# Optimization experiments

Measured on AMD Instinct MI355X. Metric: run time of the kernel, lower is better.

Reference implementation:

```python
import jax, jax.numpy as jnp
import numpy as np

N_NODES = 50000
N_EDGES = 800000
IN_CH = 128
HID = 16
HEADS = 8
OUT_CH = 40
NEG_SLOPE = 0.2  # PyG GATConv default leaky_relu slope


def segment_softmax(logits, seg, num_segments):
    # logits: [E, H], softmax over edges sharing the same destination node
    m = jax.ops.segment_max(logits, seg, num_segments=num_segments)  # [N, H]
    e = jnp.exp(logits - m[seg])
    s = jax.ops.segment_sum(e, seg, num_segments=num_segments)  # [N, H]
    return e / s[seg]


def gat_conv(x, edge_index, W, att_src, att_dst, bias, heads, ch, concat):
    N = x.shape[0]
    h = (x @ W).reshape(N, heads, ch)                     # [N, H, C]
    a_src = jnp.sum(h * att_src, axis=-1)                 # [N, H]
    a_dst = jnp.sum(h * att_dst, axis=-1)                 # [N, H]
    src, dst = edge_index[0], edge_index[1]
    alpha = jax.nn.leaky_relu(a_src[src] + a_dst[dst], NEG_SLOPE)  # [E, H]
    alpha = segment_softmax(alpha, dst, N)                # [E, H]
    msg = h[src] * alpha[:, :, None]                      # [E, H, C]
    out = jax.ops.segment_sum(msg, dst, num_segments=N)   # [N, H, C]
    out = out.reshape(N, heads * ch) if concat else out.mean(axis=1)
    return out + bias


def setup_inputs() -> dict:
    key = jax.random.key(0)
    ks = jax.random.split(key, 10)
    g = 0.1
    return {
        "x": jax.random.normal(ks[0], (N_NODES, IN_CH), jnp.float32),
        "edge_index": jax.random.randint(ks[1], (2, N_EDGES), 0, N_NODES, jnp.int32),
        "W1": jax.random.normal(ks[2], (IN_CH, HEADS * HID), jnp.float32) * g,
        "att_src1": jax.random.normal(ks[3], (HEADS, HID), jnp.float32) * g,
        "att_dst1": jax.random.normal(ks[4], (HEADS, HID), jnp.float32) * g,
        "b1": jnp.zeros((HEADS * HID,), jnp.float32),
        "W2": jax.random.normal(ks[5], (HEADS * HID, OUT_CH), jnp.float32) * g,
        "att_src2": jax.random.normal(ks[6], (1, OUT_CH), jnp.float32) * g,
        "att_dst2": jax.random.normal(ks[7], (1, OUT_CH), jnp.float32) * g,
        "b2": jnp.zeros((OUT_CH,), jnp.float32),
    }


def reference(x, edge_index, W1, att_src1, att_dst1, b1, W2, att_src2, att_dst2, b2):
    # layer 1: GATConv(in->hid, heads=8, concat) + ELU (dropout is identity in eval)
    h = gat_conv(x, edge_index, W1, att_src1, att_dst1, b1, HEADS, HID, concat=True)
    h = jax.nn.elu(h)
    # layer 2: GATConv(hid*heads->out, heads=1, concat=False)
    out = gat_conv(h, edge_index, W2, att_src2, att_dst2, b2, 1, OUT_CH, concat=False)
    return out
```

## Files before the change

kernel.cpp:

```cpp
#include <hip/hip_runtime.h>
#include <hip/hip_bf16.h>
#include <math.h>

#define N_NODES 50000
#define E_EDGES 800000
#define IN_CH 128
#define HIDX 128
#define OUT_CH 40
#define NEG_SLOPE 0.2f
#define RANK_BLKS 160
#define EDGES_PER_RANK_BLK 5000
#define GEMM_BLKS_X 782
#define PAD_SHIFT 6

static __device__ __forceinline__ unsigned int f2bf_pk(float lo, float hi) {
    unsigned int ul = __float_as_uint(lo);
    unsigned int uh = __float_as_uint(hi);
    ul = (ul + 0x7fffu + ((ul >> 16) & 1u)) >> 16;
    uh = (uh + 0x7fffu + ((uh >> 16) & 1u)) >> 16;
    return ul | (uh << 16);
}
static __device__ __forceinline__ float bf2f(unsigned short u) {
    return __uint_as_float(((unsigned int)u) << 16);
}

__global__ void zero_kernel(int* __restrict__ p, int n) {
    int i = blockIdx.x * blockDim.x + threadIdx.x;
    if (i < n) p[i] = 0;
}


__global__ __launch_bounds__(256) void gemm1_kernel(
    const float* __restrict__ x, const float* __restrict__ W1,
    const float* __restrict__ as1, const float* __restrict__ ad1,
    unsigned short* __restrict__ H1, float* __restrict__ A1s, float* __restrict__ A1d,
    const int* __restrict__ ei, int* __restrict__ deg, int* __restrict__ csr_pad)
{
    int tid = threadIdx.x;
    int bid = blockIdx.x;

    if (bid < RANK_BLKS) {
        int start = bid * EDGES_PER_RANK_BLK;
        int endv  = start + EDGES_PER_RANK_BLK;
        if (endv > E_EDGES) endv = E_EDGES;
        for (int base = start; base < endv; base += 1024) {
            int e0 = base + tid;
            int e1 = e0 + 256, e2 = e0 + 512, e3 = e0 + 768;
            bool v0 = e0 < endv, v1 = e1 < endv, v2 = e2 < endv, v3 = e3 < endv;
            int d0 = 0, d1 = 0, d2 = 0, d3 = 0;
            int s0 = 0, s1 = 0, s2 = 0, s3 = 0;
            if (v0) { d0 = ei[E_EDGES + e0]; s0 = ei[e0]; }
            if (v1) { d1 = ei[E_EDGES + e1]; s1 = ei[e1]; }
            if (v2) { d2 = ei[E_EDGES + e2]; s2 = ei[e2]; }
            if (v3) { d3 = ei[E_EDGES + e3]; s3 = ei[e3]; }
            int r0, r1, r2, r3;
            if (v0) r0 = atomicAdd(&deg[d0], 1);
            if (v1) r1 = atomicAdd(&deg[d1], 1);
            if (v2) r2 = atomicAdd(&deg[d2], 1);
            if (v3) r3 = atomicAdd(&deg[d3], 1);
            if (v0) csr_pad[(d0 << PAD_SHIFT) + r0] = s0;
            if (v1) csr_pad[(d1 << PAD_SHIFT) + r1] = s1;
            if (v2) csr_pad[(d2 << PAD_SHIFT) + r2] = s2;
            if (v3) csr_pad[(d3 << PAD_SHIFT) + r3] = s3;
        }
        return;
    }

    __shared__ float Ws[128 * 68];
    __shared__ float XT[64 * 132];
    int g = bid - RANK_BLKS;
    int rowbase = (g >> 1) * 64;
    int cb = g & 1;

    const float4* W4 = (const float4*)W1;
#pragma unroll
    for (int i = 0; i < 8; i++) {
        int f = i * 256 + tid;
        int k = f >> 4, c4 = f & 15;
        *(float4*)(Ws + k * 68 + c4 * 4) = W4[k * 32 + cb * 16 + c4];
    }
    const float4* x4 = (const float4*)x;
#pragma unroll
    for (int i = 0; i < 8; i++) {
        int f = i * 256 + tid;
        int r = f >> 5, c4 = f & 31;
        int gr = rowbase + r; if (gr >= N_NODES) gr = N_NODES - 1;
        *(float4*)(XT + r * 132 + c4 * 4) = x4[gr * 32 + c4];
    }
    __syncthreads();

    int cg = tid & 15;
    int rg = tid >> 4;
    int c0 = cg * 4;
    int r0 = rg * 4;
    float acc[4][4];
#pragma unroll
    for (int i = 0; i < 4; i++)
#pragma unroll
        for (int j = 0; j < 4; j++) acc[i][j] = 0.f;

    for (int k = 0; k < 128; k += 4) {
        float4 xv[4];
#pragma unroll
        for (int i = 0; i < 4; i++) xv[i] = *(const float4*)(XT + (r0 + i) * 132 + k);
#pragma unroll
        for (int kk = 0; kk < 4; kk++) {
            float4 wv = *(const float4*)(Ws + (k + kk) * 68 + c0);
#pragma unroll
            for (int i = 0; i < 4; i++) {
                float xs = (kk == 0) ? xv[i].x : (kk == 1) ? xv[i].y : (kk == 2) ? xv[i].z : xv[i].w;
                acc[i][0] += xs * wv.x; acc[i][1] += xs * wv.y;
                acc[i][2] += xs * wv.z; acc[i][3] += xs * wv.w;
            }
        }
    }

    int gc0 = cb * 64 + c0;
    int hh = gc0 >> 4;
    float asp[4] = {0, 0, 0, 0}, adp[4] = {0, 0, 0, 0};
#pragma unroll
    for (int j = 0; j < 4; j++) {
        float va = as1[gc0 + j];
        float vd = ad1[gc0 + j];
#pragma unroll
        for (int i = 0; i < 4; i++) { asp[i] += acc[i][j] * va; adp[i] += acc[i][j] * vd; }
    }
#pragma unroll
    for (int i = 0; i < 4; i++) {
        asp[i] += __shfl_xor(asp[i], 1); asp[i] += __shfl_xor(asp[i], 2);
        adp[i] += __shfl_xor(adp[i], 1); adp[i] += __shfl_xor(adp[i], 2);
    }
#pragma unroll
    for (int i = 0; i < 4; i++) {
        int gr = rowbase + r0 + i;
        if (gr < N_NODES) {
            uint2 v;
            v.x = f2bf_pk(acc[i][0], acc[i][1]);
            v.y = f2bf_pk(acc[i][2], acc[i][3]);
            *(uint2*)(H1 + gr * 128 + gc0) = v;
            if ((cg & 3) == 0) {
                A1s[gr * 8 + hh] = asp[i];
                A1d[gr * 8 + hh] = adp[i];
            }
        }
    }
}


__global__ __launch_bounds__(256) void agg1_kernel(
    const int* __restrict__ deg, const int* __restrict__ csr_pad,
    const float* __restrict__ A1s, const float* __restrict__ A1d,
    const unsigned short* __restrict__ H1, const float* __restrict__ b1,
    float* __restrict__ X2)
{
    int gwave = (blockIdx.x * blockDim.x + threadIdx.x) >> 6;
    int lane = threadIdx.x & 63;
    if (gwave >= N_NODES) return;
    int node = gwave;
    int beg = node << PAD_SHIFT;
    int end = beg + deg[node];
    int half = lane >> 5;
    int li = lane & 31;
    int head = li >> 2;
    int c0 = li * 4;
    float ad = A1d[node * 8 + head];
    float acc0 = 0.f, acc1 = 0.f, acc2 = 0.f, acc3 = 0.f, sumw = 0.f;
    int p = beg;
    for (; p + 16 <= end; p += 16) {
        int s[8]; float a[8]; ushort4 u[8];
#pragma unroll
        for (int t = 0; t < 8; t++) s[t] = csr_pad[p + 2 * t + half];
#pragma unroll
        for (int t = 0; t < 8; t++) a[t] = A1s[s[t] * 8 + head];
#pragma unroll
        for (int t = 0; t < 8; t++) u[t] = *(const ushort4*)(H1 + s[t] * 128 + c0);
#pragma unroll
        for (int t = 0; t < 8; t++) {
            float z = a[t] + ad; z = z >= 0.f ? z : NEG_SLOPE * z;
            float w = __expf(z);
            acc0 += w * bf2f(u[t].x);
            acc1 += w * bf2f(u[t].y);
            acc2 += w * bf2f(u[t].z);
            acc3 += w * bf2f(u[t].w);
            sumw += w;
        }
    }
    for (; p + 8 <= end; p += 8) {
        int s0 = csr_pad[p + half];
        int s1 = csr_pad[p + 2 + half];
        int s2 = csr_pad[p + 4 + half];
        int s3 = csr_pad[p + 6 + half];
        float a0 = A1s[s0 * 8 + head];
        float a1 = A1s[s1 * 8 + head];
        float a2 = A1s[s2 * 8 + head];
        float a3 = A1s[s3 * 8 + head];
        ushort4 u0 = *(const ushort4*)(H1 + s0 * 128 + c0);
        ushort4 u1 = *(const ushort4*)(H1 + s1 * 128 + c0);
        ushort4 u2 = *(const ushort4*)(H1 + s2 * 128 + c0);
        ushort4 u3 = *(const ushort4*)(H1 + s3 * 128 + c0);
        float z0 = a0 + ad; z0 = z0 >= 0.f ? z0 : NEG_SLOPE * z0; float w0 = __expf(z0);
        float z1 = a1 + ad; z1 = z1 >= 0.f ? z1 : NEG_SLOPE * z1; float w1 = __expf(z1);
        float z2 = a2 + ad; z2 = z2 >= 0.f ? z2 : NEG_SLOPE * z2; float w2 = __expf(z2);
        float z3 = a3 + ad; z3 = z3 >= 0.f ? z3 : NEG_SLOPE * z3; float w3 = __expf(z3);
        acc0 += w0 * bf2f(u0.x) + w1 * bf2f(u1.x) + w2 * bf2f(u2.x) + w3 * bf2f(u3.x);
        acc1 += w0 * bf2f(u0.y) + w1 * bf2f(u1.y) + w2 * bf2f(u2.y) + w3 * bf2f(u3.y);
        acc2 += w0 * bf2f(u0.z) + w1 * bf2f(u1.z) + w2 * bf2f(u2.z) + w3 * bf2f(u3.z);
        acc3 += w0 * bf2f(u0.w) + w1 * bf2f(u1.w) + w2 * bf2f(u2.w) + w3 * bf2f(u3.w);
        sumw += w0 + w1 + w2 + w3;
    }
    for (; p + 4 <= end; p += 4) {
        int s0 = csr_pad[p + half];
        int s1 = csr_pad[p + 2 + half];
        float a0 = A1s[s0 * 8 + head];
        float a1 = A1s[s1 * 8 + head];
        ushort4 u0 = *(const ushort4*)(H1 + s0 * 128 + c0);
        ushort4 u1 = *(const ushort4*)(H1 + s1 * 128 + c0);
        float z0 = a0 + ad; z0 = z0 >= 0.f ? z0 : NEG_SLOPE * z0; float w0 = __expf(z0);
        float z1 = a1 + ad; z1 = z1 >= 0.f ? z1 : NEG_SLOPE * z1; float w1 = __expf(z1);
        acc0 += w0 * bf2f(u0.x) + w1 * bf2f(u1.x);
        acc1 += w0 * bf2f(u0.y) + w1 * bf2f(u1.y);
        acc2 += w0 * bf2f(u0.z) + w1 * bf2f(u1.z);
        acc3 += w0 * bf2f(u0.w) + w1 * bf2f(u1.w);
        sumw += w0 + w1;
    }
    for (; p < end; p += 2) {
        int e = p + half;
        bool valid = e < end;
        int s = csr_pad[valid ? e : beg];
        float a = A1s[s * 8 + head];
        ushort4 u = *(const ushort4*)(H1 + s * 128 + c0);
        float z = a + ad; z = z >= 0.f ? z : NEG_SLOPE * z;
        float w = valid ? __expf(z) : 0.f;
        acc0 += w * bf2f(u.x);
        acc1 += w * bf2f(u.y);
        acc2 += w * bf2f(u.z);
        acc3 += w * bf2f(u.w);
        sumw += w;
    }
    acc0 += __shfl_xor(acc0, 32);
    acc1 += __shfl_xor(acc1, 32);
    acc2 += __shfl_xor(acc2, 32);
    acc3 += __shfl_xor(acc3, 32);
    sumw += __shfl_xor(sumw, 32);
    if (half == 0) {
        float inv = (end > beg) ? 1.0f / sumw : 0.0f;
        float4 bv = *(const float4*)(b1 + c0);
        float o0 = acc0 * inv + bv.x;
        float o1 = acc1 * inv + bv.y;
        float o2 = acc2 * inv + bv.z;
        float o3 = acc3 * inv + bv.w;
        o0 = o0 > 0.f ? o0 : expm1f(o0);
        o1 = o1 > 0.f ? o1 : expm1f(o1);
        o2 = o2 > 0.f ? o2 : expm1f(o2);
        o3 = o3 > 0.f ? o3 : expm1f(o3);
        float4 ov = {o0, o1, o2, o3};
        *(float4*)(X2 + node * 128 + c0) = ov;
    }
}


__global__ __launch_bounds__(256) void gemm2_kernel(
    const float* __restrict__ X2, const float* __restrict__ W2,
    const float* __restrict__ as2, const float* __restrict__ ad2,
    unsigned short* __restrict__ H2, float* __restrict__ A2s, float* __restrict__ A2d)
{
    __shared__ float Ws[128 * 40];
    __shared__ float XS[64 * 132];
    int tid = threadIdx.x;
    int rowbase = blockIdx.x * 64;

#pragma unroll
    for (int i = 0; i < 20; i++) Ws[i * 256 + tid] = W2[i * 256 + tid];

    const float4* x4 = (const float4*)X2;
#pragma unroll
    for (int i = 0; i < 8; i++) {
        int f = i * 256 + tid;
        int r = f >> 5, c4 = f & 31;
        int gr = rowbase + r; if (gr >= N_NODES) gr = N_NODES - 1;
        *(float4*)(XS + r * 132 + c4 * 4) = x4[gr * 32 + c4];
    }
    __syncthreads();

    int q = tid & 3, r = tid >> 2;
    float acc[10];
#pragma unroll
    for (int j = 0; j < 10; j++) acc[j] = 0.f;
    for (int k = 0; k < 128; k += 4) {
        float4 xv = *(const float4*)(XS + r * 132 + k);
#pragma unroll
        for (int kk = 0; kk < 4; kk++) {
            float xs = (kk == 0) ? xv.x : (kk == 1) ? xv.y : (kk == 2) ? xv.z : xv.w;
#pragma unroll
            for (int j = 0; j < 10; j++) acc[j] += xs * Ws[(k + kk) * 40 + q * 10 + j];
        }
    }
    float asum = 0.f, dsum = 0.f;
#pragma unroll
    for (int j = 0; j < 10; j++) {
        asum += acc[j] * as2[q * 10 + j];
        dsum += acc[j] * ad2[q * 10 + j];
    }
    asum += __shfl_xor(asum, 1); asum += __shfl_xor(asum, 2);
    dsum += __shfl_xor(dsum, 1); dsum += __shfl_xor(dsum, 2);
    int gr = rowbase + r;
    if (gr < N_NODES) {
#pragma unroll
        for (int t = 0; t < 5; t++)
            *(unsigned int*)(H2 + gr * 40 + q * 10 + t * 2) = f2bf_pk(acc[t * 2], acc[t * 2 + 1]);
        if (q == 0) { A2s[gr] = asum; A2d[gr] = dsum; }
    }
}


__global__ __launch_bounds__(256) void agg2_kernel(
    const int* __restrict__ deg, const int* __restrict__ csr_pad,
    const float* __restrict__ A2s, const float* __restrict__ A2d,
    const unsigned short* __restrict__ H2, const float* __restrict__ b2,
    float* __restrict__ out)
{
    int gwave = (blockIdx.x * blockDim.x + threadIdx.x) >> 6;
    int lane = threadIdx.x & 63;
    if (gwave >= N_NODES) return;
    int node = gwave;
    int beg = node << PAD_SHIFT;
    int end = beg + deg[node];
    int half = lane >> 5;
    int li = lane & 31;
    bool act = li < 20;
    int c0 = li * 2;
    int cc = act ? c0 : 0;
    float ad = A2d[node];
    float acc0 = 0.f, acc1 = 0.f, sumw = 0.f;
    int p = beg;
    for (; p + 16 <= end; p += 16) {
        int s[8]; float a[8]; ushort2 u[8];
#pragma unroll
        for (int t = 0; t < 8; t++) s[t] = csr_pad[p + 2 * t + half];
#pragma unroll
        for (int t = 0; t < 8; t++) a[t] = A2s[s[t]];
#pragma unroll
        for (int t = 0; t < 8; t++) u[t] = *(const ushort2*)(H2 + s[t] * OUT_CH + cc);
#pragma unroll
        for (int t = 0; t < 8; t++) {
            float z = a[t] + ad; z = z >= 0.f ? z : NEG_SLOPE * z;
            float w = __expf(z);
            acc0 += w * bf2f(u[t].x);
            acc1 += w * bf2f(u[t].y);
            sumw += w;
        }
    }
    for (; p + 8 <= end; p += 8) {
        int s0 = csr_pad[p + half];
        int s1 = csr_pad[p + 2 + half];
        int s2 = csr_pad[p + 4 + half];
        int s3 = csr_pad[p + 6 + half];
        float a0 = A2s[s0];
        float a1 = A2s[s1];
        float a2 = A2s[s2];
        float a3 = A2s[s3];
        ushort2 u0 = *(const ushort2*)(H2 + s0 * OUT_CH + cc);
        ushort2 u1 = *(const ushort2*)(H2 + s1 * OUT_CH + cc);
        ushort2 u2 = *(const ushort2*)(H2 + s2 * OUT_CH + cc);
        ushort2 u3 = *(const ushort2*)(H2 + s3 * OUT_CH + cc);
        float z0 = a0 + ad; z0 = z0 >= 0.f ? z0 : NEG_SLOPE * z0; float w0 = __expf(z0);
        float z1 = a1 + ad; z1 = z1 >= 0.f ? z1 : NEG_SLOPE * z1; float w1 = __expf(z1);
        float z2 = a2 + ad; z2 = z2 >= 0.f ? z2 : NEG_SLOPE * z2; float w2 = __expf(z2);
        float z3 = a3 + ad; z3 = z3 >= 0.f ? z3 : NEG_SLOPE * z3; float w3 = __expf(z3);
        acc0 += w0 * bf2f(u0.x) + w1 * bf2f(u1.x) + w2 * bf2f(u2.x) + w3 * bf2f(u3.x);
        acc1 += w0 * bf2f(u0.y) + w1 * bf2f(u1.y) + w2 * bf2f(u2.y) + w3 * bf2f(u3.y);
        sumw += w0 + w1 + w2 + w3;
    }
    for (; p + 4 <= end; p += 4) {
        int s0 = csr_pad[p + half];
        int s1 = csr_pad[p + 2 + half];
        float a0 = A2s[s0];
        float a1 = A2s[s1];
        ushort2 u0 = *(const ushort2*)(H2 + s0 * OUT_CH + cc);
        ushort2 u1 = *(const ushort2*)(H2 + s1 * OUT_CH + cc);
        float z0 = a0 + ad; z0 = z0 >= 0.f ? z0 : NEG_SLOPE * z0; float w0 = __expf(z0);
        float z1 = a1 + ad; z1 = z1 >= 0.f ? z1 : NEG_SLOPE * z1; float w1 = __expf(z1);
        acc0 += w0 * bf2f(u0.x) + w1 * bf2f(u1.x);
        acc1 += w0 * bf2f(u0.y) + w1 * bf2f(u1.y);
        sumw += w0 + w1;
    }
    for (; p < end; p += 2) {
        int e = p + half;
        bool valid = e < end;
        int s = csr_pad[valid ? e : beg];
        float a = A2s[s];
        ushort2 u = *(const ushort2*)(H2 + s * OUT_CH + cc);
        float z = a + ad; z = z >= 0.f ? z : NEG_SLOPE * z;
        float w = valid ? __expf(z) : 0.f;
        acc0 += w * bf2f(u.x);
        acc1 += w * bf2f(u.y);
        sumw += w;
    }
    acc0 += __shfl_xor(acc0, 32);
    acc1 += __shfl_xor(acc1, 32);
    sumw += __shfl_xor(sumw, 32);
    if (half == 0 && act) {
        float inv = (end > beg) ? 1.0f / sumw : 0.0f;
        float o0 = acc0 * inv + b2[c0];
        float o1 = acc1 * inv + b2[c0 + 1];
        float2 ov = {o0, o1};
        *(float2*)(out + node * OUT_CH + c0) = ov;
    }
}


extern "C" void kernel_launch(void* const* d_in, const int* in_sizes, int n_in,
                              void* d_out, int out_size, void* d_ws, size_t ws_size,
                              hipStream_t stream) {
    const float* x   = (const float*)d_in[0];
    const int*   ei  = (const int*)d_in[1];
    const float* W1  = (const float*)d_in[2];
    const float* as1 = (const float*)d_in[3];
    const float* ad1 = (const float*)d_in[4];
    const float* b1  = (const float*)d_in[5];
    const float* W2  = (const float*)d_in[6];
    const float* as2 = (const float*)d_in[7];
    const float* ad2 = (const float*)d_in[8];
    const float* b2  = (const float*)d_in[9];
    float* out = (float*)d_out;

    char* ws = (char*)d_ws;
    size_t off = 0;
    auto alloc = [&](size_t bytes) {
        void* p = ws + off;
        off += (bytes + 255) & ~size_t(255);
        return p;
    };
    unsigned short* H1 = (unsigned short*)alloc((size_t)N_NODES * 128 * 2);
    float* X2     = (float*)alloc((size_t)N_NODES * 128 * 4);
    unsigned short* H2 = (unsigned short*)alloc((size_t)N_NODES * OUT_CH * 2);
    float* A1s    = (float*)alloc((size_t)N_NODES * 8 * 4);
    float* A1d    = (float*)alloc((size_t)N_NODES * 8 * 4);
    float* A2s    = (float*)alloc((size_t)N_NODES * 4);
    float* A2d    = (float*)alloc((size_t)N_NODES * 4);
    int* deg      = (int*)alloc((size_t)N_NODES * 4);
    int* csr_pad  = (int*)alloc((size_t)N_NODES * 64 * 4);

    zero_kernel<<<(N_NODES + 255) / 256, 256, 0, stream>>>(deg, N_NODES);

    gemm1_kernel<<<RANK_BLKS + GEMM_BLKS_X * 2, 256, 0, stream>>>(
        x, W1, as1, ad1, H1, A1s, A1d, ei, deg, csr_pad);

    agg1_kernel<<<(N_NODES + 3) / 4, 256, 0, stream>>>(deg, csr_pad, A1s, A1d, H1, b1, X2);

    gemm2_kernel<<<(N_NODES + 63) / 64, 256, 0, stream>>>(X2, W2, as2, ad2, H2, A2s, A2d);
    agg2_kernel<<<(N_NODES + 3) / 4, 256, 0, stream>>>(deg, csr_pad, A2s, A2d, H2, b2, out);
}
```

Before: 225.8 us.

## Fuse layer-2 GEMM into layer-1 aggregation and double rank blocks

Folds the layer-2 projection (X2 @ W2 plus the attention dot products) into the layer-1 aggregation kernel. Each wave computes its node's ELU row into shared memory and multiplies it against a transposed W2 staged in LDS, so the fp32 X2 round trip through global memory and the separate gemm2 launch go away. Every block now loads all of W2 (20 KB) into LDS, which adds per-block load work and LDS pressure, and the per-node matvec uses only 40 of 64 lanes. Separately, the CSR-building rank phase is split across twice as many blocks with half the edges each.

```diff
diff --git a/kernel.cpp b/kernel.cpp
--- a/kernel.cpp
+++ b/kernel.cpp
@@ -8,8 +8,8 @@
 #define HIDX 128
 #define OUT_CH 40
 #define NEG_SLOPE 0.2f
-#define RANK_BLKS 160
-#define EDGES_PER_RANK_BLK 5000
+#define RANK_BLKS 320
+#define EDGES_PER_RANK_BLK 2500
 #define GEMM_BLKS_X 782
 #define PAD_SHIFT 6
 
@@ -19,6 +19,11 @@
     ul = (ul + 0x7fffu + ((ul >> 16) & 1u)) >> 16;
     uh = (uh + 0x7fffu + ((uh >> 16) & 1u)) >> 16;
     return ul | (uh << 16);
+}
+static __device__ __forceinline__ unsigned short f2bf(float v) {
+    unsigned int u = __float_as_uint(v);
+    u = (u + 0x7fffu + ((u >> 16) & 1u)) >> 16;
+    return (unsigned short)u;
 }
 static __device__ __forceinline__ float bf2f(unsigned short u) {
     return __uint_as_float(((unsigned int)u) << 16);
@@ -151,12 +156,25 @@
     const int* __restrict__ deg, const int* __restrict__ csr_pad,
     const float* __restrict__ A1s, const float* __restrict__ A1d,
     const unsigned short* __restrict__ H1, const float* __restrict__ b1,
-    float* __restrict__ X2)
+    const float* __restrict__ W2, const float* __restrict__ as2,
+    const float* __restrict__ ad2,
+    unsigned short* __restrict__ H2, float* __restrict__ A2s, float* __restrict__ A2d)
 {
-    int gwave = (blockIdx.x * blockDim.x + threadIdx.x) >> 6;
-    int lane = threadIdx.x & 63;
-    if (gwave >= N_NODES) return;
-    int node = gwave;
+    __shared__ float W2s[40 * 128];
+    __shared__ float xrow[4][128];
+    int tid = threadIdx.x;
+    int wid = tid >> 6;
+    int lane = tid & 63;
+
+#pragma unroll
+    for (int i = 0; i < 20; i++) {
+        int f = i * 256 + tid;
+        int k = f / 40, j = f - k * 40;
+        W2s[j * 128 + k] = W2[f];
+    }
+    __syncthreads();
+
+    int node = blockIdx.x * 4 + wid;
     int beg = node << PAD_SHIFT;
     int end = beg + deg[node];
     int half = lane >> 5;
@@ -242,7 +260,8 @@
     acc2 += __shfl_xor(acc2, 32);
     acc3 += __shfl_xor(acc3, 32);
     sumw += __shfl_xor(sumw, 32);
-    if (half == 0) {
+
+    {
         float inv = (end > beg) ? 1.0f / sumw : 0.0f;
         float4 bv = *(const float4*)(b1 + c0);
         float o0 = acc0 * inv + bv.x;
@@ -253,63 +272,31 @@
         o1 = o1 > 0.f ? o1 : expm1f(o1);
         o2 = o2 > 0.f ? o2 : expm1f(o2);
         o3 = o3 > 0.f ? o3 : expm1f(o3);
-        float4 ov = {o0, o1, o2, o3};
-        *(float4*)(X2 + node * 128 + c0) = ov;
-    }
-}
-
-
-__global__ __launch_bounds__(256) void gemm2_kernel(
-    const float* __restrict__ X2, const float* __restrict__ W2,
-    const float* __restrict__ as2, const float* __restrict__ ad2,
-    unsigned short* __restrict__ H2, float* __restrict__ A2s, float* __restrict__ A2d)
-{
-    __shared__ float Ws[128 * 40];
-    __shared__ float XS[64 * 132];
-    int tid = threadIdx.x;
-    int rowbase = blockIdx.x * 64;
-
-#pragma unroll
-    for (int i = 0; i < 20; i++) Ws[i * 256 + tid] = W2[i * 256 + tid];
-
-    const float4* x4 = (const float4*)X2;
-#pragma unroll
-    for (int i = 0; i < 8; i++) {
-        int f = i * 256 + tid;
-        int r = f >> 5, c4 = f & 31;
-        int gr = rowbase + r; if (gr >= N_NODES) gr = N_NODES - 1;
-        *(float4*)(XS + r * 132 + c4 * 4) = x4[gr * 32 + c4];
-    }
-    __syncthreads();
-
-    int q = tid & 3, r = tid >> 2;
-    float acc[10];
-#pragma unroll
-    for (int j = 0; j < 10; j++) acc[j] = 0.f;
-    for (int k = 0; k < 128; k += 4) {
-        float4 xv = *(const float4*)(XS + r * 132 + k);
-#pragma unroll
-        for (int kk = 0; kk < 4; kk++) {
-            float xs = (kk == 0) ? xv.x : (kk == 1) ? xv.y : (kk == 2) ? xv.z : xv.w;
-#pragma unroll
-            for (int j = 0; j < 10; j++) acc[j] += xs * Ws[(k + kk) * 40 + q * 10 + j];
-        }
-    }
-    float asum = 0.f, dsum = 0.f;
-#pragma unroll
-    for (int j = 0; j < 10; j++) {
-        asum += acc[j] * as2[q * 10 + j];
-        dsum += acc[j] * ad2[q * 10 + j];
-    }
-    asum += __shfl_xor(asum, 1); asum += __shfl_xor(asum, 2);
-    dsum += __shfl_xor(dsum, 1); dsum += __shfl_xor(dsum, 2);
-    int gr = rowbase + r;
-    if (gr < N_NODES) {
-#pragma unroll
-        for (int t = 0; t < 5; t++)
-            *(unsigned int*)(H2 + gr * 40 + q * 10 + t * 2) = f2bf_pk(acc[t * 2], acc[t * 2 + 1]);
-        if (q == 0) { A2s[gr] = asum; A2d[gr] = dsum; }
-    }
+        if (half == 0) {
+            float4 ov = {o0, o1, o2, o3};
+            *(float4*)&xrow[wid][c0] = ov;
+        }
+    }
+
+    float prodA = 0.f, prodD = 0.f;
+    if (lane < OUT_CH) {
+        float hj = 0.f;
+        const float* wj = W2s + lane * 128;
+        for (int k = 0; k < 128; k += 4) {
+            float4 xv = *(const float4*)&xrow[wid][k];
+            float4 wv = *(const float4*)(wj + k);
+            hj += xv.x * wv.x + xv.y * wv.y + xv.z * wv.z + xv.w * wv.w;
+        }
+        H2[node * OUT_CH + lane] = f2bf(hj);
+        prodA = hj * as2[lane];
+        prodD = hj * ad2[lane];
+    }
+#pragma unroll
+    for (int off = 1; off < 64; off <<= 1) {
+        prodA += __shfl_xor(prodA, off);
+        prodD += __shfl_xor(prodD, off);
+    }
+    if (lane == 0) { A2s[node] = prodA; A2d[node] = prodD; }
 }
 
 
@@ -432,7 +419,6 @@
         return p;
     };
     unsigned short* H1 = (unsigned short*)alloc((size_t)N_NODES * 128 * 2);
-    float* X2     = (float*)alloc((size_t)N_NODES * 128 * 4);
     unsigned short* H2 = (unsigned short*)alloc((size_t)N_NODES * OUT_CH * 2);
     float* A1s    = (float*)alloc((size_t)N_NODES * 8 * 4);
     float* A1d    = (float*)alloc((size_t)N_NODES * 8 * 4);
@@ -446,8 +432,8 @@
     gemm1_kernel<<<RANK_BLKS + GEMM_BLKS_X * 2, 256, 0, stream>>>(
         x, W1, as1, ad1, H1, A1s, A1d, ei, deg, csr_pad);
 
-    agg1_kernel<<<(N_NODES + 3) / 4, 256, 0, stream>>>(deg, csr_pad, A1s, A1d, H1, b1, X2);
-
-    gemm2_kernel<<<(N_NODES + 63) / 64, 256, 0, stream>>>(X2, W2, as2, ad2, H2, A2s, A2d);
+    agg1_kernel<<<N_NODES / 4, 256, 0, stream>>>(
+        deg, csr_pad, A1s, A1d, H1, b1, W2, as2, ad2, H2, A2s, A2d);
+
     agg2_kernel<<<(N_NODES + 3) / 4, 256, 0, stream>>>(deg, csr_pad, A2s, A2d, H2, b2, out);
 }
```

New measurement: 398.1 us. 1.76x slower.
